# Kernel tuning notes

Hardware: AMD Instinct MI355X
Metric: run time of the kernel (lower is better)

## Reference

```python
import jax, jax.numpy as jnp
import numpy as np

BS, LS, HS, P, M, V, D = 16, 128, 768, 8, 1024, 20000, 512
T = BS * LS
N_POS_TOTAL = 12   # pos ids >= P are non-target (copied through)
N_PRIVACY = 4      # pos ids < N_PRIVACY count as privacy terms
TEMP = 1.0


def setup_inputs() -> dict:
    key = jax.random.key(0)
    ks = jax.random.split(key, 8)
    return {
        "inp_word": jax.random.randint(ks[0], (BS, LS), 0, V),
        "inp_pos": jax.random.randint(ks[1], (BS, LS), 0, N_POS_TOTAL),
        "inp_mask": jnp.ones((BS, LS), dtype=bool),
        "ctx": jax.random.normal(ks[2], (BS, LS, HS), dtype=jnp.float32),
        "dec_W": jax.random.normal(ks[3], (P, HS, M), dtype=jnp.float32) * 0.05,
        "dec_b": jnp.zeros((P, M), dtype=jnp.float32),
        "psr_weight": jax.random.normal(ks[4], (V, D), dtype=jnp.float32) * 0.1,
        "atk_weight": jax.random.normal(ks[5], (V, D), dtype=jnp.float32) * 0.1,
        "words": jax.random.randint(ks[6], (P, M), 0, V),
        "u_gumbel": jax.random.uniform(ks[7], (T, M), dtype=jnp.float32),
    }


def reference(inp_word, inp_pos, inp_mask, ctx, dec_W, dec_b,
              psr_weight, atk_weight, words, u_gumbel):
    bs, ls = inp_word.shape
    t_tok = bs * ls
    wordf = inp_word.reshape(t_tok)          # [T]
    posf = inp_pos.reshape(t_tok)            # [T]
    ctxf = ctx.reshape(t_tok, -1)            # [T, hs]

    # per-expert decode: Linear + LogSoftmax over each expert's sub-vocab
    logits = jnp.einsum('th,phm->ptm', ctxf, dec_W) + dec_b[:, None, :]  # [P,T,M]
    pspt = jax.nn.log_softmax(logits, axis=-1)                            # [P,T,M]

    # entropy: for each POS, mean of -pspt*exp(pspt) over its masked tokens
    neg_ent = -(pspt * jnp.exp(pspt)).sum(-1)                 # [P,T]
    pm = posf[None, :] == jnp.arange(P)[:, None]              # [P,T] token->expert mask
    n_p = pm.sum(1)                                           # [P]
    ent_p = (neg_ent * pm).sum(1) / (jnp.maximum(n_p, 1) * M)
    entropy = jnp.where(n_p > 0, ent_p, 0.0).sum()

    # gumbel-softmax sample (soft), one noise draw per token
    u = jnp.clip(u_gumbel, 1e-6, 1.0 - 1e-6)
    g = -jnp.log(-jnp.log(u))                                 # [T,M]
    spt = jax.nn.softmax((pspt + g[None]) / TEMP, axis=-1)    # [P,T,M]

    # hard word choice + soft embedding mix
    idx = jnp.argmax(spt, axis=-1)                            # [P,T]
    spt_word = jnp.take_along_axis(words, idx, axis=1)        # [P,T]
    psr_lut = psr_weight[words]                               # [P,M,D]
    atk_lut = atk_weight[words]                               # [P,M,D]
    psr_e = jnp.einsum('ptm,pmd->ptd', spt, psr_lut)          # [P,T,D]
    atk_e = jnp.einsum('ptm,pmd->ptd', spt, atk_lut)          # [P,T,D]

    # combine: each token takes its own POS expert's output (scatter)
    tmask = posf < P                                          # [T] obfuscated tokens
    sel = jnp.where(tmask, posf, 0)                           # [T] expert id
    ar = jnp.arange(t_tok)
    obf_wordf = jnp.where(tmask, spt_word[sel, ar], wordf)
    obf_psr = jnp.where(tmask[:, None], psr_e[sel, ar], psr_weight[wordf])
    obf_atk = jnp.where(tmask[:, None], atk_e[sel, ar], atk_weight[wordf])

    obf_word = obf_wordf.reshape(bs, ls)
    obf_psr_emb = obf_psr.reshape(bs, ls, -1)
    obf_atk_emb = obf_atk.reshape(bs, ls, -1)
    cpy_mask = (obf_word == inp_word) & inp_mask
    obf_mask = tmask.reshape(bs, ls)
    pri_mask = (inp_pos < N_PRIVACY) & obf_mask
    ent_loss = -entropy
    return obf_word, obf_psr_emb, obf_atk_emb, ent_loss, cpy_mask, obf_mask, pri_mask
```

## Files before the change

### kernel.cpp

```cpp
#include <hip/hip_runtime.h>
#include <cstdint>

#define BSZ   16
#define LSEQ  128
#define HS    768
#define NEXP  8
#define MM    1024
#define DD    512
#define TT    (BSZ*LSEQ)
#define NPRIV 4

#define OFF_WORD 0
#define OFF_PSR  2048
#define OFF_ATK  (2048 + 2048*512)
#define OFF_ENT  (OFF_ATK + 2048*512)
#define OFF_CPY  (OFF_ENT + 1)
#define OFF_OBF  (OFF_CPY + 2048)
#define OFF_PRI  (OFF_OBF + 2048)

#define WS_SPT      0
#define WS_TOKLIST  (TT*MM*4)
#define WS_CNT      (WS_TOKLIST + NEXP*TT*4)
#define WS_ENTSUM   (WS_CNT + NEXP*4)

__global__ void k_bucket(const int* __restrict__ pos,
                         int* __restrict__ toklist, int* __restrict__ cnt)
{
  int t = blockIdx.x * blockDim.x + threadIdx.x;
  if (t >= TT) return;
  int p = pos[t];
  if (p < NEXP) {
    int r = atomicAdd(&cnt[p], 1);
    toklist[p * TT + r] = t;
  }
}

#define TM1 32
#define TN1 128
#define TK1 32
#define NSK 4

__global__ __launch_bounds__(256, 4) void k_decode(
    const float* __restrict__ ctx, const float* __restrict__ dec_W,
    const int* __restrict__ toklist, const int* __restrict__ cnt,
    float* __restrict__ logits)
{
  const int p  = blockIdx.z >> 2;
  const int ks = blockIdx.z & 3;
  const int ncnt = cnt[p];
  const int row0 = blockIdx.y * TM1;
  if (row0 >= ncnt) return;
  const int n0 = blockIdx.x * TN1;
  const int kb = ks * (HS / NSK);
  const int tid = threadIdx.x;

  __shared__ float sA[TM1][TK1 + 4];
  __shared__ float sB[TK1][TN1];

  const int tx = tid & 31, ty = tid >> 5;
  const int tx4 = tx * 4, ty4 = ty * 4;

  const int ar = tid >> 3;
  const int ac = (tid & 7) * 4;
  int tA = -1;
  if (row0 + ar < ncnt) tA = toklist[p * TT + row0 + ar];
  const float* aSrc = (tA >= 0) ? (ctx + (size_t)tA * HS + kb + ac) : nullptr;

  const int br = tid >> 5;
  const int bc4 = (tid & 31) * 4;
  const float* bSrc = dec_W + ((size_t)p * HS + kb) * MM + n0 + bc4;

  int tO[4];
  #pragma unroll
  for (int i = 0; i < 4; ++i) {
    int rr = row0 + ty4 + i;
    tO[i] = (rr < ncnt) ? toklist[p * TT + rr] : -1;
  }

  float4 aP = (tA >= 0) ? *(const float4*)aSrc : make_float4(0.f, 0.f, 0.f, 0.f);
  float4 bP0 = *(const float4*)(bSrc + (size_t)(br +  0) * MM);
  float4 bP1 = *(const float4*)(bSrc + (size_t)(br +  8) * MM);
  float4 bP2 = *(const float4*)(bSrc + (size_t)(br + 16) * MM);
  float4 bP3 = *(const float4*)(bSrc + (size_t)(br + 24) * MM);

  float acc[4][4] = {};

  for (int k0 = 0; k0 < HS / NSK; k0 += TK1) {
    *(float4*)&sA[ar][ac] = aP;
    *(float4*)&sB[br +  0][bc4] = bP0;
    *(float4*)&sB[br +  8][bc4] = bP1;
    *(float4*)&sB[br + 16][bc4] = bP2;
    *(float4*)&sB[br + 24][bc4] = bP3;
    __syncthreads();

    if (k0 + TK1 < HS / NSK) {
      const int kn = k0 + TK1;
      if (tA >= 0) aP = *(const float4*)(aSrc + kn);
      const float* bn = bSrc + (size_t)kn * MM;
      bP0 = *(const float4*)(bn + (size_t)(br +  0) * MM);
      bP1 = *(const float4*)(bn + (size_t)(br +  8) * MM);
      bP2 = *(const float4*)(bn + (size_t)(br + 16) * MM);
      bP3 = *(const float4*)(bn + (size_t)(br + 24) * MM);
    }

    #pragma unroll 8
    for (int kk = 0; kk < TK1; ++kk) {
      const float a0 = sA[ty4 + 0][kk];
      const float a1 = sA[ty4 + 1][kk];
      const float a2 = sA[ty4 + 2][kk];
      const float a3 = sA[ty4 + 3][kk];
      const float4 b = *(const float4*)&sB[kk][tx4];
      acc[0][0] = fmaf(a0, b.x, acc[0][0]); acc[0][1] = fmaf(a0, b.y, acc[0][1]);
      acc[0][2] = fmaf(a0, b.z, acc[0][2]); acc[0][3] = fmaf(a0, b.w, acc[0][3]);
      acc[1][0] = fmaf(a1, b.x, acc[1][0]); acc[1][1] = fmaf(a1, b.y, acc[1][1]);
      acc[1][2] = fmaf(a1, b.z, acc[1][2]); acc[1][3] = fmaf(a1, b.w, acc[1][3]);
      acc[2][0] = fmaf(a2, b.x, acc[2][0]); acc[2][1] = fmaf(a2, b.y, acc[2][1]);
      acc[2][2] = fmaf(a2, b.z, acc[2][2]); acc[2][3] = fmaf(a2, b.w, acc[2][3]);
      acc[3][0] = fmaf(a3, b.x, acc[3][0]); acc[3][1] = fmaf(a3, b.y, acc[3][1]);
      acc[3][2] = fmaf(a3, b.z, acc[3][2]); acc[3][3] = fmaf(a3, b.w, acc[3][3]);
    }
    __syncthreads();
  }

  #pragma unroll
  for (int i = 0; i < 4; ++i) {
    if (tO[i] >= 0) {
      float* dst = logits + (size_t)tO[i] * MM + n0 + tx4;
      atomicAdd(dst + 0, acc[i][0]);
      atomicAdd(dst + 1, acc[i][1]);
      atomicAdd(dst + 2, acc[i][2]);
      atomicAdd(dst + 3, acc[i][3]);
    }
  }
}

__device__ __forceinline__ float wred_max(float v) {
  #pragma unroll
  for (int o = 32; o > 0; o >>= 1) v = fmaxf(v, __shfl_xor(v, o));
  return v;
}
__device__ __forceinline__ float wred_sum(float v) {
  #pragma unroll
  for (int o = 32; o > 0; o >>= 1) v += __shfl_xor(v, o);
  return v;
}

__global__ __launch_bounds__(256) void k_softmax(
    const int* __restrict__ inp_word, const int* __restrict__ inp_pos,
    const int* __restrict__ inp_mask, const float* __restrict__ u_gum,
    const int* __restrict__ words, const float* __restrict__ dec_b,
    const float* __restrict__ psr_w, const float* __restrict__ atk_w,
    float* __restrict__ spt, float* __restrict__ entsum,
    float* __restrict__ out)
{
  const int t = blockIdx.x;
  const int tid = threadIdx.x;
  const int p = inp_pos[t];
  const int w_in = inp_word[t];
  const int msk = inp_mask[t];

  if (p >= NEXP) {
    if (tid < DD / 4) {
      const float4* pr = (const float4*)(psr_w + (size_t)w_in * DD);
      const float4* aw = (const float4*)(atk_w + (size_t)w_in * DD);
      ((float4*)(out + OFF_PSR + (size_t)t * DD))[tid] = pr[tid];
      ((float4*)(out + OFF_ATK + (size_t)t * DD))[tid] = aw[tid];
    }
    if (tid == 0) {
      out[OFF_WORD + t] = (float)w_in;
      out[OFF_CPY + t] = (msk != 0) ? 1.f : 0.f;
      out[OFF_OBF + t] = 0.f;
      out[OFF_PRI + t] = 0.f;
    }
    return;
  }

  float* lg = spt + (size_t)t * MM;
  const float4 l4 = *(const float4*)(lg + tid * 4);
  const float4 b4 = *(const float4*)(dec_b + (size_t)p * MM + tid * 4);
  float l[4] = {l4.x + b4.x, l4.y + b4.y, l4.z + b4.z, l4.w + b4.w};

  __shared__ float sred[4];
  __shared__ float svv[4];
  __shared__ int   svi[4];

  float v = fmaxf(fmaxf(l[0], l[1]), fmaxf(l[2], l[3]));
  v = wred_max(v);
  if ((tid & 63) == 0) sred[tid >> 6] = v;
  __syncthreads();
  const float lmax = fmaxf(fmaxf(sred[0], sred[1]), fmaxf(sred[2], sred[3]));

  float e[4], ls = 0.f;
  #pragma unroll
  for (int j = 0; j < 4; ++j) { e[j] = expf(l[j] - lmax); ls += e[j]; }
  ls = wred_sum(ls);
  __syncthreads();
  if ((tid & 63) == 0) sred[tid >> 6] = ls;
  __syncthreads();
  const float s1 = sred[0] + sred[1] + sred[2] + sred[3];
  const float lse = logf(s1);

  float pe = 0.f;
  #pragma unroll
  for (int j = 0; j < 4; ++j) pe += (l[j] - lmax - lse) * e[j];
  pe = wred_sum(pe);
  __syncthreads();
  if ((tid & 63) == 0) sred[tid >> 6] = pe;
  __syncthreads();
  if (tid == 0) {
    const float tot = (sred[0] + sred[1] + sred[2] + sred[3]) / s1;
    atomicAdd(&entsum[p], -tot);
  }

  const float4 u4 = *(const float4*)(u_gum + (size_t)t * MM + tid * 4);
  float uu[4] = {u4.x, u4.y, u4.z, u4.w};
  float z[4];
  #pragma unroll
  for (int j = 0; j < 4; ++j) {
    float u = fminf(fmaxf(uu[j], 1e-6f), 1.0f - 1e-6f);
    z[j] = l[j] - logf(-logf(u));
  }

  float zv = z[0]; int zi = tid * 4;
  #pragma unroll
  for (int j = 1; j < 4; ++j) { if (z[j] > zv) { zv = z[j]; zi = tid * 4 + j; } }
  #pragma unroll
  for (int o = 32; o > 0; o >>= 1) {
    float ov = __shfl_xor(zv, o);
    int   oi = __shfl_xor(zi, o);
    if (ov > zv || (ov == zv && oi < zi)) { zv = ov; zi = oi; }
  }
  if ((tid & 63) == 0) { svv[tid >> 6] = zv; svi[tid >> 6] = zi; }
  __syncthreads();
  float fv = svv[0]; int fi = svi[0];
  #pragma unroll
  for (int q = 1; q < 4; ++q) {
    if (svv[q] > fv || (svv[q] == fv && svi[q] < fi)) { fv = svv[q]; fi = svi[q]; }
  }

  float e2[4], ls2 = 0.f;
  #pragma unroll
  for (int j = 0; j < 4; ++j) { e2[j] = expf(z[j] - fv); ls2 += e2[j]; }
  ls2 = wred_sum(ls2);
  __syncthreads();
  if ((tid & 63) == 0) sred[tid >> 6] = ls2;
  __syncthreads();
  const float s2 = sred[0] + sred[1] + sred[2] + sred[3];

  float4 o4;
  o4.x = e2[0] / s2; o4.y = e2[1] / s2; o4.z = e2[2] / s2; o4.w = e2[3] / s2;
  *(float4*)(lg + tid * 4) = o4;

  if (tid == 0) {
    const int wsel = words[p * MM + fi];
    out[OFF_WORD + t] = (float)wsel;
    out[OFF_CPY + t] = ((wsel == w_in) && (msk != 0)) ? 1.f : 0.f;
    out[OFF_OBF + t] = 1.f;
    out[OFF_PRI + t] = (p < NPRIV) ? 1.f : 0.f;
  }
}

#define TM3 32
#define TN3 64
#define TK3 32
#define NSM 4

__global__ __launch_bounds__(256, 4) void k_embed(
    const float* __restrict__ spt, const int* __restrict__ words,
    const float* __restrict__ psr_w, const float* __restrict__ atk_w,
    const int* __restrict__ toklist, const int* __restrict__ cnt,
    float* __restrict__ out)
{
  const int p  = blockIdx.z >> 2;
  const int ms = blockIdx.z & 3;
  const int ncnt = cnt[p];
  const int row0 = blockIdx.y * TM3;
  if (row0 >= ncnt) return;
  const int n0 = blockIdx.x * TN3;
  const int mb = ms * (MM / NSM);
  const int tid = threadIdx.x;

  __shared__ float sS[TM3][TK3 + 4];
  __shared__ float sL[2][TK3][68];

  const int tx = tid & 15, ty = tid >> 4;
  const int tx4 = tx * 4, ty2 = ty * 2;

  const int ar = tid >> 3;
  const int ac = (tid & 7) * 4;
  int tS = -1;
  if (row0 + ar < ncnt) tS = toklist[p * TT + row0 + ar];
  const float* sSrc = (tS >= 0) ? (spt + (size_t)tS * MM + mb + ac) : nullptr;

  const int lr = tid >> 4;
  const int lc4 = (tid & 15) * 4;
  const int* wRow = words + p * MM + mb + lr;

  int tO[2];
  #pragma unroll
  for (int i = 0; i < 2; ++i) {
    int rr = row0 + ty2 + i;
    tO[i] = (rr < ncnt) ? toklist[p * TT + rr] : -1;
  }

  float4 sP = (tS >= 0) ? *(const float4*)sSrc : make_float4(0.f, 0.f, 0.f, 0.f);
  int w0 = wRow[0], w1 = wRow[16];
  float4 lp0 = *(const float4*)(psr_w + (size_t)w0 * DD + n0 + lc4);
  float4 lp1 = *(const float4*)(psr_w + (size_t)w1 * DD + n0 + lc4);
  float4 la0 = *(const float4*)(atk_w + (size_t)w0 * DD + n0 + lc4);
  float4 la1 = *(const float4*)(atk_w + (size_t)w1 * DD + n0 + lc4);

  float ap[2][4] = {};
  float aa[2][4] = {};

  for (int m0 = 0; m0 < MM / NSM; m0 += TK3) {
    *(float4*)&sS[ar][ac] = sP;
    *(float4*)&sL[0][lr +  0][lc4] = lp0;
    *(float4*)&sL[0][lr + 16][lc4] = lp1;
    *(float4*)&sL[1][lr +  0][lc4] = la0;
    *(float4*)&sL[1][lr + 16][lc4] = la1;
    __syncthreads();

    if (m0 + TK3 < MM / NSM) {
      const int mn = m0 + TK3;
      if (tS >= 0) sP = *(const float4*)(sSrc + mn);
      w0 = wRow[mn]; w1 = wRow[mn + 16];
      lp0 = *(const float4*)(psr_w + (size_t)w0 * DD + n0 + lc4);
      lp1 = *(const float4*)(psr_w + (size_t)w1 * DD + n0 + lc4);
      la0 = *(const float4*)(atk_w + (size_t)w0 * DD + n0 + lc4);
      la1 = *(const float4*)(atk_w + (size_t)w1 * DD + n0 + lc4);
    }

    #pragma unroll 8
    for (int kk = 0; kk < TK3; ++kk) {
      const float s0 = sS[ty2 + 0][kk];
      const float s1 = sS[ty2 + 1][kk];
      const float4 pv = *(const float4*)&sL[0][kk][tx4];
      const float4 av = *(const float4*)&sL[1][kk][tx4];
      ap[0][0] = fmaf(s0, pv.x, ap[0][0]); ap[0][1] = fmaf(s0, pv.y, ap[0][1]);
      ap[0][2] = fmaf(s0, pv.z, ap[0][2]); ap[0][3] = fmaf(s0, pv.w, ap[0][3]);
      ap[1][0] = fmaf(s1, pv.x, ap[1][0]); ap[1][1] = fmaf(s1, pv.y, ap[1][1]);
      ap[1][2] = fmaf(s1, pv.z, ap[1][2]); ap[1][3] = fmaf(s1, pv.w, ap[1][3]);
      aa[0][0] = fmaf(s0, av.x, aa[0][0]); aa[0][1] = fmaf(s0, av.y, aa[0][1]);
      aa[0][2] = fmaf(s0, av.z, aa[0][2]); aa[0][3] = fmaf(s0, av.w, aa[0][3]);
      aa[1][0] = fmaf(s1, av.x, aa[1][0]); aa[1][1] = fmaf(s1, av.y, aa[1][1]);
      aa[1][2] = fmaf(s1, av.z, aa[1][2]); aa[1][3] = fmaf(s1, av.w, aa[1][3]);
    }
    __syncthreads();
  }

  #pragma unroll
  for (int i = 0; i < 2; ++i) {
    if (tO[i] >= 0) {
      float* dp = out + OFF_PSR + (size_t)tO[i] * DD + n0 + tx4;
      float* da = out + OFF_ATK + (size_t)tO[i] * DD + n0 + tx4;
      atomicAdd(dp + 0, ap[i][0]); atomicAdd(dp + 1, ap[i][1]);
      atomicAdd(dp + 2, ap[i][2]); atomicAdd(dp + 3, ap[i][3]);
      atomicAdd(da + 0, aa[i][0]); atomicAdd(da + 1, aa[i][1]);
      atomicAdd(da + 2, aa[i][2]); atomicAdd(da + 3, aa[i][3]);
    }
  }
}

__global__ void k_finalize(const float* __restrict__ entsum,
                           const int* __restrict__ cnt, float* __restrict__ out)
{
  if (threadIdx.x == 0 && blockIdx.x == 0) {
    float s = 0.f;
    for (int p = 0; p < NEXP; ++p) {
      int n = cnt[p];
      if (n > 0) s += entsum[p] / ((float)n * (float)MM);
    }
    out[OFF_ENT] = -s;
  }
}

extern "C" void kernel_launch(void* const* d_in, const int* in_sizes, int n_in,
                              void* d_out, int out_size, void* d_ws, size_t ws_size,
                              hipStream_t stream)
{
  (void)in_sizes; (void)n_in; (void)out_size; (void)ws_size;

  const int*   inp_word = (const int*)d_in[0];
  const int*   inp_pos  = (const int*)d_in[1];
  const int*   inp_mask = (const int*)d_in[2];
  const float* ctx      = (const float*)d_in[3];
  const float* dec_W    = (const float*)d_in[4];
  const float* dec_b    = (const float*)d_in[5];
  const float* psr_w    = (const float*)d_in[6];
  const float* atk_w    = (const float*)d_in[7];
  const int*   words    = (const int*)d_in[8];
  const float* u_gum    = (const float*)d_in[9];

  float* out = (float*)d_out;
  char*  ws  = (char*)d_ws;
  float* spt     = (float*)(ws + WS_SPT);
  int*   toklist = (int*)(ws + WS_TOKLIST);
  int*   cnt     = (int*)(ws + WS_CNT);
  float* entsum  = (float*)(ws + WS_ENTSUM);

  hipMemsetAsync(ws + WS_CNT, 0, NEXP * 4 * 2, stream);
  hipMemsetAsync(spt, 0, (size_t)TT * MM * 4, stream);
  hipMemsetAsync(out + OFF_PSR, 0, (size_t)2 * 2048 * 512 * 4, stream);

  k_bucket<<<TT / 256, 256, 0, stream>>>(inp_pos, toklist, cnt);
  k_decode<<<dim3(MM / TN1, TT / TM1, NEXP * NSK), 256, 0, stream>>>(
      ctx, dec_W, toklist, cnt, spt);
  k_softmax<<<TT, 256, 0, stream>>>(
      inp_word, inp_pos, inp_mask, u_gum, words, dec_b, psr_w, atk_w, spt, entsum, out);
  k_embed<<<dim3(DD / TN3, TT / TM3, NEXP * NSM), 256, 0, stream>>>(
      spt, words, psr_w, atk_w, toklist, cnt, out);
  k_finalize<<<1, 64, 0, stream>>>(entsum, cnt, out);
}
```

Measured before the change: 375.5 us.

## Enlarge row tiles to 128 with 8x8 register blocking in decode and embed GEMMs

Both grouped GEMM kernels now use 128-token row tiles, with each thread computing an 8x8 output block. The A operand is stored transposed in shared memory so each k-step reads contiguous rows. This raises weight reuse and FMA-to-load ratio, cutting shared and global traffic per FLOP. In exchange it uses more registers (occupancy hint lowered to 2), wastes more work on partially filled tail tiles, and leaves fewer blocks in the grid.

```diff
diff --git a/kernel.cpp b/kernel.cpp
--- a/kernel.cpp
+++ b/kernel.cpp
@@ -35,12 +35,12 @@
   }
 }
 
-#define TM1 32
+#define TM1 128
 #define TN1 128
 #define TK1 32
 #define NSK 4
 
-__global__ __launch_bounds__(256, 4) void k_decode(
+__global__ __launch_bounds__(256, 2) void k_decode(
     const float* __restrict__ ctx, const float* __restrict__ dec_W,
     const int* __restrict__ toklist, const int* __restrict__ cnt,
     float* __restrict__ logits)
@@ -54,82 +54,99 @@
   const int kb = ks * (HS / NSK);
   const int tid = threadIdx.x;
 
-  __shared__ float sA[TM1][TK1 + 4];
-  __shared__ float sB[TK1][TN1];
-
-  const int tx = tid & 31, ty = tid >> 5;
-  const int tx4 = tx * 4, ty4 = ty * 4;
-
-  const int ar = tid >> 3;
-  const int ac = (tid & 7) * 4;
-  int tA = -1;
-  if (row0 + ar < ncnt) tA = toklist[p * TT + row0 + ar];
-  const float* aSrc = (tA >= 0) ? (ctx + (size_t)tA * HS + kb + ac) : nullptr;
-
-  const int br = tid >> 5;
-  const int bc4 = (tid & 31) * 4;
-  const float* bSrc = dec_W + ((size_t)p * HS + kb) * MM + n0 + bc4;
-
-  int tO[4];
-  #pragma unroll
-  for (int i = 0; i < 4; ++i) {
-    int rr = row0 + ty4 + i;
-    tO[i] = (rr < ncnt) ? toklist[p * TT + rr] : -1;
-  }
-
-  float4 aP = (tA >= 0) ? *(const float4*)aSrc : make_float4(0.f, 0.f, 0.f, 0.f);
-  float4 bP0 = *(const float4*)(bSrc + (size_t)(br +  0) * MM);
-  float4 bP1 = *(const float4*)(bSrc + (size_t)(br +  8) * MM);
-  float4 bP2 = *(const float4*)(bSrc + (size_t)(br + 16) * MM);
-  float4 bP3 = *(const float4*)(bSrc + (size_t)(br + 24) * MM);
-
-  float acc[4][4] = {};
+  __shared__ float sA[TK1][TM1 + 4];
+  __shared__ float sB[TK1][TN1 + 4];
+
+  const int sRow = tid >> 1;
+  const int sHalf = (tid & 1) * 16;
+  int tS = -1;
+  if (row0 + sRow < ncnt) tS = toklist[p * TT + row0 + sRow];
+  const float* aSrc = (tS >= 0) ? (ctx + (size_t)tS * HS + kb + sHalf) : nullptr;
+
+  const int bR = tid >> 3;
+  const int bC = (tid & 7) * 16;
+  const float* bBase = dec_W + (size_t)(p * HS + kb) * MM + n0 + bC;
+
+  const int tx = tid & 15, ty = tid >> 4;
+  const int tx4 = tx * 4;
+  const int ty8 = ty * 8;
+
+  float4 aP0, aP1, aP2, aP3, bP0, bP1, bP2, bP3;
+  if (tS >= 0) {
+    aP0 = *(const float4*)(aSrc + 0);  aP1 = *(const float4*)(aSrc + 4);
+    aP2 = *(const float4*)(aSrc + 8);  aP3 = *(const float4*)(aSrc + 12);
+  } else {
+    aP0 = aP1 = aP2 = aP3 = make_float4(0.f, 0.f, 0.f, 0.f);
+  }
+  {
+    const float* b0 = bBase + (size_t)bR * MM;
+    bP0 = *(const float4*)(b0 + 0);  bP1 = *(const float4*)(b0 + 4);
+    bP2 = *(const float4*)(b0 + 8);  bP3 = *(const float4*)(b0 + 12);
+  }
+
+  float4 acc0[8], acc1[8];
+  #pragma unroll
+  for (int r = 0; r < 8; ++r) {
+    acc0[r] = make_float4(0.f, 0.f, 0.f, 0.f);
+    acc1[r] = make_float4(0.f, 0.f, 0.f, 0.f);
+  }
 
   for (int k0 = 0; k0 < HS / NSK; k0 += TK1) {
-    *(float4*)&sA[ar][ac] = aP;
-    *(float4*)&sB[br +  0][bc4] = bP0;
-    *(float4*)&sB[br +  8][bc4] = bP1;
-    *(float4*)&sB[br + 16][bc4] = bP2;
-    *(float4*)&sB[br + 24][bc4] = bP3;
+    sA[sHalf +  0][sRow] = aP0.x; sA[sHalf +  1][sRow] = aP0.y;
+    sA[sHalf +  2][sRow] = aP0.z; sA[sHalf +  3][sRow] = aP0.w;
+    sA[sHalf +  4][sRow] = aP1.x; sA[sHalf +  5][sRow] = aP1.y;
+    sA[sHalf +  6][sRow] = aP1.z; sA[sHalf +  7][sRow] = aP1.w;
+    sA[sHalf +  8][sRow] = aP2.x; sA[sHalf +  9][sRow] = aP2.y;
+    sA[sHalf + 10][sRow] = aP2.z; sA[sHalf + 11][sRow] = aP2.w;
+    sA[sHalf + 12][sRow] = aP3.x; sA[sHalf + 13][sRow] = aP3.y;
+    sA[sHalf + 14][sRow] = aP3.z; sA[sHalf + 15][sRow] = aP3.w;
+    *(float4*)&sB[bR][bC +  0] = bP0;
+    *(float4*)&sB[bR][bC +  4] = bP1;
+    *(float4*)&sB[bR][bC +  8] = bP2;
+    *(float4*)&sB[bR][bC + 12] = bP3;
     __syncthreads();
 
     if (k0 + TK1 < HS / NSK) {
       const int kn = k0 + TK1;
-      if (tA >= 0) aP = *(const float4*)(aSrc + kn);
-      const float* bn = bSrc + (size_t)kn * MM;
-      bP0 = *(const float4*)(bn + (size_t)(br +  0) * MM);
-      bP1 = *(const float4*)(bn + (size_t)(br +  8) * MM);
-      bP2 = *(const float4*)(bn + (size_t)(br + 16) * MM);
-      bP3 = *(const float4*)(bn + (size_t)(br + 24) * MM);
+      if (tS >= 0) {
+        aP0 = *(const float4*)(aSrc + kn + 0);  aP1 = *(const float4*)(aSrc + kn + 4);
+        aP2 = *(const float4*)(aSrc + kn + 8);  aP3 = *(const float4*)(aSrc + kn + 12);
+      }
+      const float* bn = bBase + (size_t)(kn + bR) * MM;
+      bP0 = *(const float4*)(bn + 0);  bP1 = *(const float4*)(bn + 4);
+      bP2 = *(const float4*)(bn + 8);  bP3 = *(const float4*)(bn + 12);
     }
 
     #pragma unroll 8
     for (int kk = 0; kk < TK1; ++kk) {
-      const float a0 = sA[ty4 + 0][kk];
-      const float a1 = sA[ty4 + 1][kk];
-      const float a2 = sA[ty4 + 2][kk];
-      const float a3 = sA[ty4 + 3][kk];
-      const float4 b = *(const float4*)&sB[kk][tx4];
-      acc[0][0] = fmaf(a0, b.x, acc[0][0]); acc[0][1] = fmaf(a0, b.y, acc[0][1]);
-      acc[0][2] = fmaf(a0, b.z, acc[0][2]); acc[0][3] = fmaf(a0, b.w, acc[0][3]);
-      acc[1][0] = fmaf(a1, b.x, acc[1][0]); acc[1][1] = fmaf(a1, b.y, acc[1][1]);
-      acc[1][2] = fmaf(a1, b.z, acc[1][2]); acc[1][3] = fmaf(a1, b.w, acc[1][3]);
-      acc[2][0] = fmaf(a2, b.x, acc[2][0]); acc[2][1] = fmaf(a2, b.y, acc[2][1]);
-      acc[2][2] = fmaf(a2, b.z, acc[2][2]); acc[2][3] = fmaf(a2, b.w, acc[2][3]);
-      acc[3][0] = fmaf(a3, b.x, acc[3][0]); acc[3][1] = fmaf(a3, b.y, acc[3][1]);
-      acc[3][2] = fmaf(a3, b.z, acc[3][2]); acc[3][3] = fmaf(a3, b.w, acc[3][3]);
+      const float4 b0 = *(const float4*)&sB[kk][tx4];
+      const float4 b1 = *(const float4*)&sB[kk][tx4 + 64];
+      #pragma unroll
+      for (int rr = 0; rr < 8; ++rr) {
+        const float a = sA[kk][ty8 + rr];
+        acc0[rr].x = fmaf(a, b0.x, acc0[rr].x);
+        acc0[rr].y = fmaf(a, b0.y, acc0[rr].y);
+        acc0[rr].z = fmaf(a, b0.z, acc0[rr].z);
+        acc0[rr].w = fmaf(a, b0.w, acc0[rr].w);
+        acc1[rr].x = fmaf(a, b1.x, acc1[rr].x);
+        acc1[rr].y = fmaf(a, b1.y, acc1[rr].y);
+        acc1[rr].z = fmaf(a, b1.z, acc1[rr].z);
+        acc1[rr].w = fmaf(a, b1.w, acc1[rr].w);
+      }
     }
     __syncthreads();
   }
 
   #pragma unroll
-  for (int i = 0; i < 4; ++i) {
-    if (tO[i] >= 0) {
-      float* dst = logits + (size_t)tO[i] * MM + n0 + tx4;
-      atomicAdd(dst + 0, acc[i][0]);
-      atomicAdd(dst + 1, acc[i][1]);
-      atomicAdd(dst + 2, acc[i][2]);
-      atomicAdd(dst + 3, acc[i][3]);
+  for (int rr = 0; rr < 8; ++rr) {
+    const int gr = row0 + ty8 + rr;
+    if (gr < ncnt) {
+      const int tok = toklist[p * TT + gr];
+      float* dst = logits + (size_t)tok * MM + n0 + tx4;
+      atomicAdd(dst +  0, acc0[rr].x); atomicAdd(dst +  1, acc0[rr].y);
+      atomicAdd(dst +  2, acc0[rr].z); atomicAdd(dst +  3, acc0[rr].w);
+      atomicAdd(dst + 64, acc1[rr].x); atomicAdd(dst + 65, acc1[rr].y);
+      atomicAdd(dst + 66, acc1[rr].z); atomicAdd(dst + 67, acc1[rr].w);
     }
   }
 }
@@ -260,12 +277,12 @@
   }
 }
 
-#define TM3 32
+#define TM3 128
 #define TN3 64
 #define TK3 32
 #define NSM 4
 
-__global__ __launch_bounds__(256, 4) void k_embed(
+__global__ __launch_bounds__(256, 2) void k_embed(
     const float* __restrict__ spt, const int* __restrict__ words,
     const float* __restrict__ psr_w, const float* __restrict__ atk_w,
     const int* __restrict__ toklist, const int* __restrict__ cnt,
@@ -280,84 +297,102 @@
   const int mb = ms * (MM / NSM);
   const int tid = threadIdx.x;
 
-  __shared__ float sS[TM3][TK3 + 4];
+  __shared__ float sS[TK3][TM3 + 4];
   __shared__ float sL[2][TK3][68];
 
+  const int sRow = tid >> 1;
+  const int sHalf = (tid & 1) * 16;
+  int tS = -1;
+  if (row0 + sRow < ncnt) tS = toklist[p * TT + row0 + sRow];
+  const float* sSrc = (tS >= 0) ? (spt + (size_t)tS * MM + mb + sHalf) : nullptr;
+
+  const int g = tid >> 4;
+  const int l4 = (tid & 15) * 4;
+  const int* wB = words + p * MM + mb;
+
   const int tx = tid & 15, ty = tid >> 4;
-  const int tx4 = tx * 4, ty2 = ty * 2;
-
-  const int ar = tid >> 3;
-  const int ac = (tid & 7) * 4;
-  int tS = -1;
-  if (row0 + ar < ncnt) tS = toklist[p * TT + row0 + ar];
-  const float* sSrc = (tS >= 0) ? (spt + (size_t)tS * MM + mb + ac) : nullptr;
-
-  const int lr = tid >> 4;
-  const int lc4 = (tid & 15) * 4;
-  const int* wRow = words + p * MM + mb + lr;
-
-  int tO[2];
-  #pragma unroll
-  for (int i = 0; i < 2; ++i) {
-    int rr = row0 + ty2 + i;
-    tO[i] = (rr < ncnt) ? toklist[p * TT + rr] : -1;
-  }
-
-  float4 sP = (tS >= 0) ? *(const float4*)sSrc : make_float4(0.f, 0.f, 0.f, 0.f);
-  int w0 = wRow[0], w1 = wRow[16];
-  float4 lp0 = *(const float4*)(psr_w + (size_t)w0 * DD + n0 + lc4);
-  float4 lp1 = *(const float4*)(psr_w + (size_t)w1 * DD + n0 + lc4);
-  float4 la0 = *(const float4*)(atk_w + (size_t)w0 * DD + n0 + lc4);
-  float4 la1 = *(const float4*)(atk_w + (size_t)w1 * DD + n0 + lc4);
-
-  float ap[2][4] = {};
-  float aa[2][4] = {};
+  const int tx4 = tx * 4;
+  const int ty8 = ty * 8;
+
+  float4 sP0, sP1, sP2, sP3;
+  if (tS >= 0) {
+    sP0 = *(const float4*)(sSrc + 0);  sP1 = *(const float4*)(sSrc + 4);
+    sP2 = *(const float4*)(sSrc + 8);  sP3 = *(const float4*)(sSrc + 12);
+  } else {
+    sP0 = sP1 = sP2 = sP3 = make_float4(0.f, 0.f, 0.f, 0.f);
+  }
+  int w0 = wB[g], w1 = wB[g + 16];
+  float4 lp0 = *(const float4*)(psr_w + (size_t)w0 * DD + n0 + l4);
+  float4 lp1 = *(const float4*)(psr_w + (size_t)w1 * DD + n0 + l4);
+  float4 la0 = *(const float4*)(atk_w + (size_t)w0 * DD + n0 + l4);
+  float4 la1 = *(const float4*)(atk_w + (size_t)w1 * DD + n0 + l4);
+
+  float4 accP[8], accA[8];
+  #pragma unroll
+  for (int r = 0; r < 8; ++r) {
+    accP[r] = make_float4(0.f, 0.f, 0.f, 0.f);
+    accA[r] = make_float4(0.f, 0.f, 0.f, 0.f);
+  }
 
   for (int m0 = 0; m0 < MM / NSM; m0 += TK3) {
-    *(float4*)&sS[ar][ac] = sP;
-    *(float4*)&sL[0][lr +  0][lc4] = lp0;
-    *(float4*)&sL[0][lr + 16][lc4] = lp1;
-    *(float4*)&sL[1][lr +  0][lc4] = la0;
-    *(float4*)&sL[1][lr + 16][lc4] = la1;
+    sS[sHalf +  0][sRow] = sP0.x; sS[sHalf +  1][sRow] = sP0.y;
+    sS[sHalf +  2][sRow] = sP0.z; sS[sHalf +  3][sRow] = sP0.w;
+    sS[sHalf +  4][sRow] = sP1.x; sS[sHalf +  5][sRow] = sP1.y;
+    sS[sHalf +  6][sRow] = sP1.z; sS[sHalf +  7][sRow] = sP1.w;
+    sS[sHalf +  8][sRow] = sP2.x; sS[sHalf +  9][sRow] = sP2.y;
+    sS[sHalf + 10][sRow] = sP2.z; sS[sHalf + 11][sRow] = sP2.w;
+    sS[sHalf + 12][sRow] = sP3.x; sS[sHalf + 13][sRow] = sP3.y;
+    sS[sHalf + 14][sRow] = sP3.z; sS[sHalf + 15][sRow] = sP3.w;
+    *(float4*)&sL[0][g +  0][l4] = lp0;
+    *(float4*)&sL[0][g + 16][l4] = lp1;
+    *(float4*)&sL[1][g +  0][l4] = la0;
+    *(float4*)&sL[1][g + 16][l4] = la1;
     __syncthreads();
 
     if (m0 + TK3 < MM / NSM) {
       const int mn = m0 + TK3;
-      if (tS >= 0) sP = *(const float4*)(sSrc + mn);
-      w0 = wRow[mn]; w1 = wRow[mn + 16];
-      lp0 = *(const float4*)(psr_w + (size_t)w0 * DD + n0 + lc4);
-      lp1 = *(const float4*)(psr_w + (size_t)w1 * DD + n0 + lc4);
-      la0 = *(const float4*)(atk_w + (size_t)w0 * DD + n0 + lc4);
-      la1 = *(const float4*)(atk_w + (size_t)w1 * DD + n0 + lc4);
+      if (tS >= 0) {
+        sP0 = *(const float4*)(sSrc + mn + 0);  sP1 = *(const float4*)(sSrc + mn + 4);
+        sP2 = *(const float4*)(sSrc + mn + 8);  sP3 = *(const float4*)(sSrc + mn + 12);
+      }
+      w0 = wB[mn + g]; w1 = wB[mn + g + 16];
+      lp0 = *(const float4*)(psr_w + (size_t)w0 * DD + n0 + l4);
+      lp1 = *(const float4*)(psr_w + (size_t)w1 * DD + n0 + l4);
+      la0 = *(const float4*)(atk_w + (size_t)w0 * DD + n0 + l4);
+      la1 = *(const float4*)(atk_w + (size_t)w1 * DD + n0 + l4);
     }
 
     #pragma unroll 8
     for (int kk = 0; kk < TK3; ++kk) {
-      const float s0 = sS[ty2 + 0][kk];
-      const float s1 = sS[ty2 + 1][kk];
       const float4 pv = *(const float4*)&sL[0][kk][tx4];
       const float4 av = *(const float4*)&sL[1][kk][tx4];
-      ap[0][0] = fmaf(s0, pv.x, ap[0][0]); ap[0][1] = fmaf(s0, pv.y, ap[0][1]);
-      ap[0][2] = fmaf(s0, pv.z, ap[0][2]); ap[0][3] = fmaf(s0, pv.w, ap[0][3]);
-      ap[1][0] = fmaf(s1, pv.x, ap[1][0]); ap[1][1] = fmaf(s1, pv.y, ap[1][1]);
-      ap[1][2] = fmaf(s1, pv.z, ap[1][2]); ap[1][3] = fmaf(s1, pv.w, ap[1][3]);
-      aa[0][0] = fmaf(s0, av.x, aa[0][0]); aa[0][1] = fmaf(s0, av.y, aa[0][1]);
-      aa[0][2] = fmaf(s0, av.z, aa[0][2]); aa[0][3] = fmaf(s0, av.w, aa[0][3]);
-      aa[1][0] = fmaf(s1, av.x, aa[1][0]); aa[1][1] = fmaf(s1, av.y, aa[1][1]);
-      aa[1][2] = fmaf(s1, av.z, aa[1][2]); aa[1][3] = fmaf(s1, av.w, aa[1][3]);
+      #pragma unroll
+      for (int rr = 0; rr < 8; ++rr) {
+        const float s = sS[kk][ty8 + rr];
+        accP[rr].x = fmaf(s, pv.x, accP[rr].x);
+        accP[rr].y = fmaf(s, pv.y, accP[rr].y);
+        accP[rr].z = fmaf(s, pv.z, accP[rr].z);
+        accP[rr].w = fmaf(s, pv.w, accP[rr].w);
+        accA[rr].x = fmaf(s, av.x, accA[rr].x);
+        accA[rr].y = fmaf(s, av.y, accA[rr].y);
+        accA[rr].z = fmaf(s, av.z, accA[rr].z);
+        accA[rr].w = fmaf(s, av.w, accA[rr].w);
+      }
     }
     __syncthreads();
   }
 
   #pragma unroll
-  for (int i = 0; i < 2; ++i) {
-    if (tO[i] >= 0) {
-      float* dp = out + OFF_PSR + (size_t)tO[i] * DD + n0 + tx4;
-      float* da = out + OFF_ATK + (size_t)tO[i] * DD + n0 + tx4;
-      atomicAdd(dp + 0, ap[i][0]); atomicAdd(dp + 1, ap[i][1]);
-      atomicAdd(dp + 2, ap[i][2]); atomicAdd(dp + 3, ap[i][3]);
-      atomicAdd(da + 0, aa[i][0]); atomicAdd(da + 1, aa[i][1]);
-      atomicAdd(da + 2, aa[i][2]); atomicAdd(da + 3, aa[i][3]);
+  for (int rr = 0; rr < 8; ++rr) {
+    const int gr = row0 + ty8 + rr;
+    if (gr < ncnt) {
+      const int tok = toklist[p * TT + gr];
+      float* dp = out + OFF_PSR + (size_t)tok * DD + n0 + tx4;
+      float* da = out + OFF_ATK + (size_t)tok * DD + n0 + tx4;
+      atomicAdd(dp + 0, accP[rr].x); atomicAdd(dp + 1, accP[rr].y);
+      atomicAdd(dp + 2, accP[rr].z); atomicAdd(dp + 3, accP[rr].w);
+      atomicAdd(da + 0, accA[rr].x); atomicAdd(da + 1, accA[rr].y);
+      atomicAdd(da + 2, accA[rr].z); atomicAdd(da + 3, accA[rr].w);
     }
   }
 }
```

Measured after the change: 430.0 us. +14.5%, slower.
